# Performance work log

Hardware: AMD Instinct MI355X
Metric: run time of the kernel (lower is better)

Reference implementation:

```python
import jax, jax.numpy as jnp
import numpy as np

B, L, D, H, NB = 8, 256, 128, 4, 2
HD = D // H
N_ITEMS, TIME_SPAN = 50000, 256
EPS = 1e-8
NEG = -(2.0 ** 32) + 1.0  # torch uses -2**32+1 padding value


def _ln(x, g, b):
    m = jnp.mean(x, -1, keepdims=True)
    v = jnp.mean((x - m) ** 2, -1, keepdims=True)
    return (x - m) / jnp.sqrt(v + EPS) * g + b


def setup_inputs() -> dict:
    ks = iter(jax.random.split(jax.random.key(0), 40))

    def nrm(shape, s=0.02):
        return jax.random.normal(next(ks), shape, jnp.float32) * s

    inp = {
        "user_ids": jax.random.randint(next(ks), (B,), 0, 1000),
        "log_seqs": jax.random.randint(next(ks), (B, L), 0, N_ITEMS + 1),
        "time_matrices": jax.random.randint(next(ks), (B, L, L), 0, TIME_SPAN + 1),
        "pos_seqs": jax.random.randint(next(ks), (B, L), 1, N_ITEMS + 1),
        "neg_seqs": jax.random.randint(next(ks), (B, L), 1, N_ITEMS + 1),
    }
    inp["item_emb"] = nrm((N_ITEMS + 1, D)).at[0].set(0.0)  # padding_idx=0
    inp["posK_emb"] = nrm((L, D))
    inp["posV_emb"] = nrm((L, D))
    inp["timeK_emb"] = nrm((TIME_SPAN + 1, D))
    inp["timeV_emb"] = nrm((TIME_SPAN + 1, D))
    inp["ln1_g"] = jnp.ones((NB, D)); inp["ln1_b"] = jnp.zeros((NB, D))
    inp["Wq"] = nrm((NB, D, D)); inp["bq"] = jnp.zeros((NB, D))
    inp["Wk"] = nrm((NB, D, D)); inp["bk"] = jnp.zeros((NB, D))
    inp["Wv"] = nrm((NB, D, D)); inp["bv"] = jnp.zeros((NB, D))
    inp["ln2_g"] = jnp.ones((NB, D)); inp["ln2_b"] = jnp.zeros((NB, D))
    inp["W1"] = nrm((NB, D, D)); inp["b1"] = jnp.zeros((NB, D))
    inp["W2"] = nrm((NB, D, D)); inp["b2"] = jnp.zeros((NB, D))
    inp["lnf_g"] = jnp.ones((D,)); inp["lnf_b"] = jnp.zeros((D,))
    return inp


def reference(user_ids, log_seqs, time_matrices, pos_seqs, neg_seqs,
              item_emb, posK_emb, posV_emb, timeK_emb, timeV_emb,
              ln1_g, ln1_b, Wq, bq, Wk, bk, Wv, bv, ln2_g, ln2_b,
              W1, b1, W2, b2, lnf_g, lnf_b):
    # dropout layers are identity in eval mode
    seqs = item_emb[log_seqs] * jnp.sqrt(jnp.float32(D))          # [B,L,D]
    tK = timeK_emb[time_matrices].reshape(B, L, L, H, HD)          # [B,Lq,Lk,H,hd]
    tV = timeV_emb[time_matrices].reshape(B, L, L, H, HD)
    pad = log_seqs == 0                                            # [B,L]
    seqs = seqs * (~pad)[..., None]
    causal = jnp.triu(jnp.ones((L, L), bool), 1)                   # ~tril -> masked
    # time_mask masks by QUERY position (matches torch unsqueeze(-1).expand)
    mask = pad[:, None, :, None] | causal[None, None]              # [B,1,Lq,Lk]
    posKh = posK_emb.reshape(L, H, HD)
    posVh = posV_emb.reshape(L, H, HD)
    for i in range(NB):
        q_in = _ln(seqs, ln1_g[i], ln1_b[i])
        Qh = (q_in @ Wq[i] + bq[i]).reshape(B, L, H, HD).transpose(0, 2, 1, 3)
        Kh = (seqs @ Wk[i] + bk[i]).reshape(B, L, H, HD).transpose(0, 2, 1, 3)
        Vh = (seqs @ Wv[i] + bv[i]).reshape(B, L, H, HD).transpose(0, 2, 1, 3)
        scores = jnp.einsum("bhqd,bhkd->bhqk", Qh, Kh)
        scores = scores + jnp.einsum("bhqd,khd->bhqk", Qh, posKh)
        scores = scores + jnp.einsum("bqkhd,bhqd->bhqk", tK, Qh)
        scores = scores / jnp.sqrt(jnp.float32(HD))
        scores = jnp.where(mask, NEG, scores)
        A = jax.nn.softmax(scores, axis=-1)                        # [B,H,Lq,Lk]
        out = jnp.einsum("bhqk,bhkd->bhqd", A, Vh)
        out = out + jnp.einsum("bhqk,khd->bhqd", A, posVh)
        out = out + jnp.einsum("bhqk,bqkhd->bhqd", A, tV)
        out = out.transpose(0, 2, 1, 3).reshape(B, L, D)
        seqs = q_in + out                                          # residual on Q
        seqs = _ln(seqs, ln2_g[i], ln2_b[i])
        h = jax.nn.relu(seqs @ W1[i] + b1[i])                      # conv1d k=1 == linear
        seqs = seqs + (h @ W2[i] + b2[i])
        seqs = seqs * (~pad)[..., None]
    feats = _ln(seqs, lnf_g, lnf_b)
    pos_logits = jnp.sum(feats * item_emb[pos_seqs], -1)           # [B,L]
    neg_logits = jnp.sum(feats * item_emb[neg_seqs], -1)
    return (pos_logits, neg_logits)
```

## Files before the change

### kernel.cpp

```cpp
#include <hip/hip_runtime.h>
#include <hip/hip_bf16.h>

#define L_ 256
#define H_ 4
#define ROWS 2048
#define NEGV (-4294967295.0f)

typedef unsigned short us16;

__device__ __forceinline__ float us2f(us16 u){ return __uint_as_float(((unsigned)u)<<16); }
__device__ __forceinline__ us16 f2us(float f){ __hip_bfloat16 h=__float2bfloat16(f); return *(us16*)&h; }

__device__ __forceinline__ float dot2bf(unsigned x, unsigned y, float c){
#if __has_builtin(__builtin_amdgcn_fdot2_f32_bf16)
    typedef __bf16 bf2 __attribute__((ext_vector_type(2)));
    union U{ unsigned u; bf2 v; };
    U ux, uy; ux.u=x; uy.u=y;
    return __builtin_amdgcn_fdot2_f32_bf16(ux.v, uy.v, c, false);
#else
    float r=fmaf(us2f((us16)(x&0xffffu)), us2f((us16)(y&0xffffu)), c);
    return fmaf(us2f((us16)(x>>16)), us2f((us16)(y>>16)), r);
#endif
}

struct KArgs {
    const int *log_seqs, *tmat, *pos_seqs, *neg_seqs;
    const float *item_emb, *posK, *posV, *timeK, *timeV;
    const float *ln1g, *ln1b, *bq, *bk, *bv, *ln2g, *ln2b, *b1, *b2, *lnfg, *lnfb;
    const float *Wq, *Wk, *Wv, *W1, *W2;
    float *qin0, *qin1, *out;
    unsigned *wsP;
    us16 *tmK, *tmV, *Qb0, *Kb0, *Vb0, *Qb1, *Kb1, *Vb1;
};

__device__ __forceinline__ float gemv32(const unsigned* __restrict__ wp,
                                        const unsigned* __restrict__ xp, int c, int hk){
    float s0=0.f, s1=0.f;
    int base=hk*32;
    #pragma unroll 8
    for(int j=0;j<32;j+=2){
        s0=dot2bf(xp[base+j],   wp[(size_t)(base+j)*128+c],   s0);
        s1=dot2bf(xp[base+j+1], wp[(size_t)(base+j+1)*128+c], s1);
    }
    return s0+s1;
}

__device__ __forceinline__ void ln_rows(float* sA,
        const float* __restrict__ g, const float* __restrict__ b,
        float* qin_out, int r0, int tid){
    int r=tid>>5, l=tid&31;
    float* x=sA+r*128;
    float x0=x[l],x1=x[l+32],x2=x[l+64],x3=x[l+96];
    float s=x0+x1+x2+x3;
    #pragma unroll
    for(int o=16;o;o>>=1) s+=__shfl_xor(s,o,64);
    float m=s*(1.f/128.f);
    float d0=x0-m,d1=x1-m,d2=x2-m,d3=x3-m;
    float v=d0*d0+d1*d1+d2*d2+d3*d3;
    #pragma unroll
    for(int o=16;o;o>>=1) v+=__shfl_xor(v,o,64);
    float rstd=rsqrtf(v*(1.f/128.f)+1e-8f);
    float y0=d0*rstd*g[l]+b[l];
    float y1=d1*rstd*g[l+32]+b[l+32];
    float y2=d2*rstd*g[l+64]+b[l+64];
    float y3=d3*rstd*g[l+96]+b[l+96];
    x[l]=y0; x[l+32]=y1; x[l+64]=y2; x[l+96]=y3;
    if(qin_out){
        float* q=qin_out+(size_t)(r0+r)*128;
        q[l]=y0; q[l+32]=y1; q[l+64]=y2; q[l+96]=y3;
    }
}

__global__ __launch_bounds__(256) void k_pre(KArgs a){
    __shared__ __align__(16) float sA[1024];
    int tid=threadIdx.x, bid=blockIdx.x;
    if(bid<768){
        int m=bid>>8, rg=bid&255, r0=rg*8;
        {
            int rl=tid>>5, c4=tid&31;
            int id=a.log_seqs[r0+rl];
            float4 v=((const float4*)a.item_emb)[id*32+c4];
            float sc = id? 11.3137085f : 0.f;
            v.x*=sc; v.y*=sc; v.z*=sc; v.w*=sc;
            ((float4*)sA)[tid]=v;
        }
        __syncthreads();
        if(m==0){ ln_rows(sA, a.ln1g, a.ln1b, a.qin0, r0, tid); __syncthreads(); }
        const float* Wsrc=(m==0)?a.Wq:(m==1)?a.Wk:a.Wv;
        int cp=tid&63, rp=tid>>6, c0=2*cp, ra=2*rp, rb=ra+1;
        float a00=0,a01=0,a10=0,a11=0;
        const float* Ar=sA+ra*128;
        const float* Br=sA+rb*128;
        #pragma unroll 8
        for(int kk=0;kk<128;kk++){
            float2 wp=((const float2*)(Wsrc+(size_t)kk*128))[cp];
            float x0=Ar[kk], x1=Br[kk];
            a00=fmaf(x0,wp.x,a00); a01=fmaf(x0,wp.y,a01);
            a10=fmaf(x1,wp.x,a10); a11=fmaf(x1,wp.y,a11);
        }
        int r_a=r0+ra, r_b=r0+rb;
        if(m==0){
            float b0v=a.bq[c0], b1v=a.bq[c0+1];
            ushort2 s0; s0.x=f2us(a00+b0v); s0.y=f2us(a01+b1v);
            ushort2 s1; s1.x=f2us(a10+b0v); s1.y=f2us(a11+b1v);
            *(ushort2*)(a.Qb0+(size_t)r_a*128+c0)=s0;
            *(ushort2*)(a.Qb0+(size_t)r_b*128+c0)=s1;
        } else if(m==1){
            float b0v=a.bk[c0], b1v=a.bk[c0+1];
            int qa=r_a&255, qb2=r_b&255;
            ushort2 s0; s0.x=f2us(a00+b0v+a.posK[qa*128+c0]);  s0.y=f2us(a01+b1v+a.posK[qa*128+c0+1]);
            ushort2 s1; s1.x=f2us(a10+b0v+a.posK[qb2*128+c0]); s1.y=f2us(a11+b1v+a.posK[qb2*128+c0+1]);
            *(ushort2*)(a.Kb0+(size_t)r_a*128+c0)=s0;
            *(ushort2*)(a.Kb0+(size_t)r_b*128+c0)=s1;
        } else {
            float b0v=a.bv[c0], b1v=a.bv[c0+1];
            int qa=r_a&255, qb2=r_b&255;
            unsigned lo0=f2us(a00+b0v+a.posV[qa*128+c0]);
            unsigned lo1=f2us(a01+b1v+a.posV[qa*128+c0+1]);
            unsigned hi0=f2us(a10+b0v+a.posV[qb2*128+c0]);
            unsigned hi1=f2us(a11+b1v+a.posV[qb2*128+c0+1]);
            unsigned* Vo=(unsigned*)a.Vb0+((size_t)r_a>>1)*128;
            Vo[c0]  =lo0|(hi0<<16);
            Vo[c0+1]=lo1|(hi1<<16);
        }
    } else if(bid<880){
        int j=bid-768; int m=j>>4; int sub=j&15;
        const float* base;
        switch(m){
            case 0: base=a.W1; break;        case 1: base=a.W2; break;
            case 2: base=a.Wq+16384; break;  case 3: base=a.Wk+16384; break;
            case 4: base=a.Wv+16384; break;  case 5: base=a.W1+16384; break;
            default: base=a.W2+16384; break;
        }
        unsigned* dst=a.wsP+(size_t)m*8192;
        #pragma unroll
        for(int t2=0;t2<2;t2++){
            int o=sub*512+t2*256+tid;
            int kp=o>>7, c=o&127;
            unsigned lo=f2us(base[(size_t)(2*kp)*128+c]);
            unsigned hi=f2us(base[(size_t)(2*kp+1)*128+c]);
            dst[o]=lo|(hi<<16);
        }
    } else {
        int gi=(bid-880)*256+tid;
        if(gi<8224){
            float4 v=((const float4*)a.timeK)[gi];
            ushort4 o; o.x=f2us(v.x);o.y=f2us(v.y);o.z=f2us(v.z);o.w=f2us(v.w);
            ((ushort4*)a.tmK)[gi]=o;
        } else if(gi<16448){
            int g2=gi-8224;
            float4 v=((const float4*)a.timeV)[g2];
            ushort4 o; o.x=f2us(v.x);o.y=f2us(v.y);o.z=f2us(v.z);o.w=f2us(v.w);
            ((ushort4*)a.tmV)[g2]=o;
        }
    }
}

__global__ __launch_bounds__(512,4) void k_blk(KArgs a, int layer){
    __shared__ __align__(16) char uni[16448];
    __shared__ __align__(16) unsigned sAb[8*128];
    __shared__ __align__(16) int      sTM[512];
    __shared__ __align__(16) unsigned sQb[128];
    __shared__ __align__(16) float    sX[256];
    __shared__ __align__(16) unsigned sXb[128];
    __shared__ __align__(16) unsigned sHb[128];
    __shared__ __align__(16) unsigned sYb[128];
    __shared__ float sRed[4], sRed2[4], sRB[8];
    float* sS =(float*)uni;
    float* sPj=(float*)(uni+8192);
    float* sPr=(float*)uni;
    float* sG0=(float*)uni;
    float* sG1=(float*)(uni+2048);

    int tid=threadIdx.x, bid=blockIdx.x;
    int b=bid>>7, p=bid&127;
    int q1=p, q2=255-p, b0=b*L_;
    int r1=b0+q1, r2=b0+q2;
    bool pad1=a.log_seqs[r1]==0, pad2=a.log_seqs[r2]==0;
    const us16* Qb = layer? a.Qb1:a.Qb0;
    const us16* Kb = layer? a.Kb1:a.Kb0;
    const unsigned* Vbu = (const unsigned*)(layer? a.Vb1:a.Vb0);
    const float* qin = layer? a.qin1:a.qin0;
    const float scale=0.17677669529663687f;

    if(tid<128){
        int rowq=tid>>6, j=tid&63;
        int r=rowq?r2:r1;
        sQb[rowq*64+j]=((const unsigned*)Qb)[(size_t)r*64+j];
    }
    if(tid<256) sTM[tid]=a.tmat[(size_t)r1*L_+tid];
    else        sTM[tid]=a.tmat[(size_t)r2*L_+(tid-256)];
    __syncthreads();

    {
        int ch=tid&15, h=ch>>2;
        uint4 qv0=((const uint4*)(sQb))[ch];
        uint4 qv1=((const uint4*)(sQb+64))[ch];
        for(int t=tid>>4; t<257; t+=32){
            uint4 tv=((const uint4*)(a.tmK+(size_t)t*128))[ch];
            float p0=0.f,p1=0.f;
            p0=dot2bf(qv0.x,tv.x,p0); p0=dot2bf(qv0.y,tv.y,p0);
            p0=dot2bf(qv0.z,tv.z,p0); p0=dot2bf(qv0.w,tv.w,p0);
            p1=dot2bf(qv1.x,tv.x,p1); p1=dot2bf(qv1.y,tv.y,p1);
            p1=dot2bf(qv1.z,tv.z,p1); p1=dot2bf(qv1.w,tv.w,p1);
            p0+=__shfl_xor(p0,1,64); p0+=__shfl_xor(p0,2,64);
            p1+=__shfl_xor(p1,1,64); p1+=__shfl_xor(p1,2,64);
            if((ch&3)==0){
                sPj[t*4+h]       =p0;
                sPj[1028+t*4+h]  =p1;
            }
        }
    }
    __syncthreads();

    {
        int k=tid&255, i2=tid>>8;
        const uint4* K4=(const uint4*)(Kb+(size_t)(b0+k)*128);
        int qq=i2?q2:q1; bool pad=i2?pad2:pad1;
        int tm=sTM[i2*256+k];
        bool act=(k<=qq)&&!pad;
        float o0=NEGV,o1=NEGV,o2=NEGV,o3=NEGV;
        if(act){
            const uint4* Q4=(const uint4*)(sQb+i2*64);
            float4 pj=((const float4*)sPj)[i2*257+tm];
            float r4[4];
            #pragma unroll
            for(int h=0;h<4;h++){
                uint4 k0=K4[h*4+0],k1=K4[h*4+1],k2=K4[h*4+2],k3=K4[h*4+3];
                uint4 qa=Q4[h*4+0],qb=Q4[h*4+1],qc=Q4[h*4+2],qd=Q4[h*4+3];
                float s0=0,s1=0;
                s0=dot2bf(qa.x,k0.x,s0); s1=dot2bf(qa.y,k0.y,s1);
                s0=dot2bf(qa.z,k0.z,s0); s1=dot2bf(qa.w,k0.w,s1);
                s0=dot2bf(qb.x,k1.x,s0); s1=dot2bf(qb.y,k1.y,s1);
                s0=dot2bf(qb.z,k1.z,s0); s1=dot2bf(qb.w,k1.w,s1);
                s0=dot2bf(qc.x,k2.x,s0); s1=dot2bf(qc.y,k2.y,s1);
                s0=dot2bf(qc.z,k2.z,s0); s1=dot2bf(qc.w,k2.w,s1);
                s0=dot2bf(qd.x,k3.x,s0); s1=dot2bf(qd.y,k3.y,s1);
                s0=dot2bf(qd.z,k3.z,s0); s1=dot2bf(qd.w,k3.w,s1);
                r4[h]=s0+s1;
            }
            o0=(r4[0]+pj.x)*scale; o1=(r4[1]+pj.y)*scale;
            o2=(r4[2]+pj.z)*scale; o3=(r4[3]+pj.w)*scale;
        }
        sS[(i2*4+0)*256+k]=o0; sS[(i2*4+1)*256+k]=o1;
        sS[(i2*4+2)*256+k]=o2; sS[(i2*4+3)*256+k]=o3;
    }
    __syncthreads();

    {
        int w=tid>>6, lane=tid&63;
        int i2=w>>2, h=w&3;
        const float* row=sS+(i2*4+h)*256;
        float v0=row[lane],v1=row[lane+64],v2=row[lane+128],v3=row[lane+192];
        float mm=fmaxf(fmaxf(v0,v1),fmaxf(v2,v3));
        #pragma unroll
        for(int o=32;o;o>>=1) mm=fmaxf(mm,__shfl_xor(mm,o,64));
        float e0=__expf(v0-mm),e1=__expf(v1-mm),e2=__expf(v2-mm),e3=__expf(v3-mm);
        float ss=e0+e1+e2+e3;
        #pragma unroll
        for(int o=32;o;o>>=1) ss+=__shfl_xor(ss,o,64);
        float inv=1.f/ss;
        us16* ar=((us16*)sAb)+(i2*4+h)*256;
        ar[lane]    =f2us(e0*inv); ar[lane+64] =f2us(e1*inv);
        ar[lane+128]=f2us(e2*inv); ar[lane+192]=f2us(e3*inv);
    }
    __syncthreads();

    {
        int i2=tid>>8, s8=(tid>>4)&15, dq=tid&15;
        int qq=i2?q2:q1; bool pad=i2?pad2:pad1;
        int kend=pad?L_:qq+1;
        int k0=s8*16;
        int kmax=kend-k0; kmax=kmax<0?0:(kmax>16?16:kmax);
        int npair=(kmax+1)>>1;
        const unsigned* arow=sAb+(i2*4+(dq>>2))*128;
        const int* tmrow=sTM+i2*256;
        float ac0=0,ac1=0,ac2=0,ac3=0,ac4=0,ac5=0,ac6=0,ac7=0;
        for(int kp=0;kp<npair;kp++){
            int kx=k0+2*kp;
            unsigned aa=arow[kx>>1];
            int tma=tmrow[kx], tmb=tmrow[kx+1];
            const uint4* Vp=(const uint4*)(Vbu+((size_t)(b0+kx)>>1)*128+dq*8);
            uint4 va=Vp[0], vb4=Vp[1];
            uint4 ta=((const uint4*)(a.tmV+(size_t)tma*128))[dq];
            uint4 tb=((const uint4*)(a.tmV+(size_t)tmb*128))[dq];
            ac0=dot2bf(aa,va.x,ac0);  ac1=dot2bf(aa,va.y,ac1);
            ac2=dot2bf(aa,va.z,ac2);  ac3=dot2bf(aa,va.w,ac3);
            ac4=dot2bf(aa,vb4.x,ac4); ac5=dot2bf(aa,vb4.y,ac5);
            ac6=dot2bf(aa,vb4.z,ac6); ac7=dot2bf(aa,vb4.w,ac7);
            unsigned p0=__builtin_amdgcn_perm(tb.x,ta.x,0x05040100u);
            unsigned p1=__builtin_amdgcn_perm(tb.x,ta.x,0x07060302u);
            unsigned p2=__builtin_amdgcn_perm(tb.y,ta.y,0x05040100u);
            unsigned p3=__builtin_amdgcn_perm(tb.y,ta.y,0x07060302u);
            unsigned p4=__builtin_amdgcn_perm(tb.z,ta.z,0x05040100u);
            unsigned p5=__builtin_amdgcn_perm(tb.z,ta.z,0x07060302u);
            unsigned p6=__builtin_amdgcn_perm(tb.w,ta.w,0x05040100u);
            unsigned p7=__builtin_amdgcn_perm(tb.w,ta.w,0x07060302u);
            ac0=dot2bf(aa,p0,ac0); ac1=dot2bf(aa,p1,ac1);
            ac2=dot2bf(aa,p2,ac2); ac3=dot2bf(aa,p3,ac3);
            ac4=dot2bf(aa,p4,ac4); ac5=dot2bf(aa,p5,ac5);
            ac6=dot2bf(aa,p6,ac6); ac7=dot2bf(aa,p7,ac7);
        }
        float* dst=sPr+(i2*16+s8)*128+dq*8;
        ((float4*)dst)[0]=make_float4(ac0,ac1,ac2,ac3);
        ((float4*)dst)[1]=make_float4(ac4,ac5,ac6,ac7);
    }
    __syncthreads();

    int ii=tid>>7&1, l=tid&127;
    float v=0.f, d2v=0.f;
    if(tid<256){
        v=qin[(size_t)(ii?r2:r1)*128+l];
        #pragma unroll
        for(int sl=0;sl<16;sl++) v+=sPr[(ii*16+sl)*128+l];
        float s=v;
        #pragma unroll
        for(int o=32;o;o>>=1) s+=__shfl_xor(s,o,64);
        if((tid&63)==0) sRed[ii*2+((tid>>6)&1)]=s;
    }
    __syncthreads();
    if(tid<256){
        float m=(sRed[ii*2]+sRed[ii*2+1])*(1.f/128.f);
        d2v=v-m;
        float vv=d2v*d2v;
        #pragma unroll
        for(int o=32;o;o>>=1) vv+=__shfl_xor(vv,o,64);
        if((tid&63)==0) sRed2[ii*2+((tid>>6)&1)]=vv;
    }
    __syncthreads();
    if(tid<256){
        float rstd=rsqrtf((sRed2[ii*2]+sRed2[ii*2+1])*(1.f/128.f)+1e-8f);
        float y=d2v*rstd*a.ln2g[layer*128+l]+a.ln2b[layer*128+l];
        sX[ii*128+l]=y;
        ((us16*)sXb)[ii*128+l]=f2us(y);
    }
    __syncthreads();

    int c=tid&127, iw=(tid>>7)&1, hk=tid>>8;
    bool padw = iw? pad2:pad1;
    int  rrw  = iw? r2:r1;
    int  qw   = iw? q2:q1;
    sG0[tid]=gemv32(a.wsP+(size_t)(layer?5:0)*8192, sXb+iw*64, c, hk);
    __syncthreads();
    if(hk==0){
        float h1=sG0[tid]+sG0[tid+256]+a.b1[layer*128+c];
        ((us16*)sHb)[iw*128+c]=f2us(fmaxf(h1,0.f));
    }
    __syncthreads();
    sG1[tid]=gemv32(a.wsP+(size_t)(layer?6:1)*8192, sHb+iw*64, c, hk);
    __syncthreads();
    float f=0.f;
    if(hk==0){
        f=sG1[tid]+sG1[tid+256]+a.b2[layer*128+c]+sX[iw*128+c];
        if(padw) f=0.f;
    }

    if(layer==0){
        float d=0.f;
        if(hk==0){
            ((us16*)sYb)[iw*128+c]=f2us(f);
            float s=f;
            #pragma unroll
            for(int o=32;o;o>>=1) s+=__shfl_xor(s,o,64);
            if((tid&63)==0) sRB[iw*2+((tid>>6)&1)]=s;
        }
        __syncthreads();
        if(hk==0){
            float m=(sRB[iw*2]+sRB[iw*2+1])*(1.f/128.f);
            d=f-m;
            float vv=d*d;
            #pragma unroll
            for(int o=32;o;o>>=1) vv+=__shfl_xor(vv,o,64);
            if((tid&63)==0) sRB[4+iw*2+((tid>>6)&1)]=vv;
        }
        __syncthreads();
        if(hk==0){
            float rstd=rsqrtf((sRB[4+iw*2]+sRB[5+iw*2])*(1.f/128.f)+1e-8f);
            float y1=d*rstd*a.ln1g[128+c]+a.ln1b[128+c];
            a.qin1[(size_t)rrw*128+c]=y1;
            ((us16*)sXb)[iw*128+c]=f2us(y1);
        }
        __syncthreads();
        sG0[tid]=gemv32(a.wsP+(size_t)2*8192, sXb+iw*64, c, hk);
        __syncthreads();
        if(hk==0) a.Qb1[(size_t)rrw*128+c]=f2us(sG0[tid]+sG0[tid+256]+a.bq[128+c]);
        sG1[tid]=gemv32(a.wsP+(size_t)3*8192, sYb+iw*64, c, hk);
        __syncthreads();
        if(hk==0) a.Kb1[(size_t)rrw*128+c]=f2us(sG1[tid]+sG1[tid+256]+a.bk[128+c]+a.posK[qw*128+c]);
        sG0[tid]=gemv32(a.wsP+(size_t)4*8192, sYb+iw*64, c, hk);
        __syncthreads();
        if(hk==0) ((us16*)a.Vb1)[((size_t)rrw>>1)*256+2*c+(rrw&1)]
                    =f2us(sG0[tid]+sG0[tid+256]+a.bv[128+c]+a.posV[qw*128+c]);
    } else {
        float d=0.f;
        if(hk==0){
            float s=f;
            #pragma unroll
            for(int o=32;o;o>>=1) s+=__shfl_xor(s,o,64);
            if((tid&63)==0) sRB[iw*2+((tid>>6)&1)]=s;
        }
        __syncthreads();
        if(hk==0){
            float m=(sRB[iw*2]+sRB[iw*2+1])*(1.f/128.f);
            d=f-m;
            float vv=d*d;
            #pragma unroll
            for(int o=32;o;o>>=1) vv+=__shfl_xor(vv,o,64);
            if((tid&63)==0) sRB[4+iw*2+((tid>>6)&1)]=vv;
        }
        __syncthreads();
        if(hk==0){
            float rstd=rsqrtf((sRB[4+iw*2]+sRB[5+iw*2])*(1.f/128.f)+1e-8f);
            sX[iw*128+c]=d*rstd*a.lnfg[c]+a.lnfb[c];
        }
        __syncthreads();
        int w=tid>>6, lane=tid&63;
        if(w<4){
            int rowi=w>>1, neg=w&1;
            int rg = rowi? r2:r1;
            int id = neg? a.neg_seqs[rg] : a.pos_seqs[rg];
            const float* e=a.item_emb+(size_t)id*128;
            float s2 = sX[rowi*128+lane]*e[lane] + sX[rowi*128+lane+64]*e[lane+64];
            #pragma unroll
            for(int o=32;o;o>>=1) s2+=__shfl_xor(s2,o,64);
            if(lane==0) a.out[neg*ROWS+rg]=s2;
        }
    }
}

extern "C" void kernel_launch(void* const* d_in, const int* in_sizes, int n_in,
                              void* d_out, int out_size, void* d_ws, size_t ws_size,
                              hipStream_t stream) {
    KArgs a;
    a.log_seqs=(const int*)d_in[1];
    a.tmat    =(const int*)d_in[2];
    a.pos_seqs=(const int*)d_in[3];
    a.neg_seqs=(const int*)d_in[4];
    a.item_emb=(const float*)d_in[5];
    a.posK =(const float*)d_in[6];
    a.posV =(const float*)d_in[7];
    a.timeK=(const float*)d_in[8];
    a.timeV=(const float*)d_in[9];
    a.ln1g=(const float*)d_in[10];
    a.ln1b=(const float*)d_in[11];
    a.Wq=(const float*)d_in[12];
    a.bq=(const float*)d_in[13];
    a.Wk=(const float*)d_in[14];
    a.bk=(const float*)d_in[15];
    a.Wv=(const float*)d_in[16];
    a.bv=(const float*)d_in[17];
    a.ln2g=(const float*)d_in[18];
    a.ln2b=(const float*)d_in[19];
    a.W1=(const float*)d_in[20];
    a.b1=(const float*)d_in[21];
    a.W2=(const float*)d_in[22];
    a.b2=(const float*)d_in[23];
    a.lnfg=(const float*)d_in[24];
    a.lnfb=(const float*)d_in[25];

    const size_t MB=1u<<20;
    char* w=(char*)d_ws;
    a.qin0=(float*)(w+0*MB);
    a.qin1=(float*)(w+1*MB);
    a.Qb0 =(us16*) (w+2*MB);
    a.Kb0 =(us16*) (w+2*MB+512*1024);
    a.Vb0 =(us16*) (w+3*MB);
    a.Qb1 =(us16*) (w+3*MB+512*1024);
    a.Kb1 =(us16*) (w+4*MB);
    a.Vb1 =(us16*) (w+4*MB+512*1024);
    a.wsP =(unsigned*)(w+5*MB);
    a.tmK =(us16*) (w+5*MB+256*1024);
    a.tmV =(us16*) (w+5*MB+384*1024);
    a.out =(float*)d_out;

    k_pre<<<946,256,0,stream>>>(a);
    k_blk<<<1024,512,0,stream>>>(a,0);
    k_blk<<<1024,512,0,stream>>>(a,1);
}
```

Baseline: 206.6 us.

## Process one query row per block instead of paired causal rows

The attention/FFN block kernel now handles a single query row per 256-thread block (2048 blocks) instead of pairing rows q and 255-q in 512-thread blocks (1024 blocks). Shared memory per block halves and launch bounds move to 256x8, which should allow more resident blocks and drop the pairing index logic. In exchange the causal load balance that pairing gave is lost, so blocks for early rows finish quickly while late rows do full work. Per-row reloads of the time-K projection table also double across the grid.

After: 215.3 us. 1.04x slower.

```diff
diff --git a/kernel.cpp b/kernel.cpp
--- a/kernel.cpp
+++ b/kernel.cpp
@@ -156,73 +156,58 @@
     }
 }
 
-__global__ __launch_bounds__(512,4) void k_blk(KArgs a, int layer){
-    __shared__ __align__(16) char uni[16448];
-    __shared__ __align__(16) unsigned sAb[8*128];
-    __shared__ __align__(16) int      sTM[512];
-    __shared__ __align__(16) unsigned sQb[128];
-    __shared__ __align__(16) float    sX[256];
-    __shared__ __align__(16) unsigned sXb[128];
-    __shared__ __align__(16) unsigned sHb[128];
-    __shared__ __align__(16) unsigned sYb[128];
-    __shared__ float sRed[4], sRed2[4], sRB[8];
+__global__ __launch_bounds__(256,8) void k_blk(KArgs a, int layer){
+    __shared__ __align__(16) char uni[8224];
+    __shared__ __align__(16) unsigned sAb[4*128];
+    __shared__ __align__(16) int      sTM[256];
+    __shared__ __align__(16) unsigned sQb[64];
+    __shared__ __align__(16) float    sX[128];
+    __shared__ __align__(16) unsigned sXb[64];
+    __shared__ __align__(16) unsigned sHb[64];
+    __shared__ __align__(16) unsigned sYb[64];
+    __shared__ float sRed[2], sRed2[2], sRB[4];
     float* sS =(float*)uni;
-    float* sPj=(float*)(uni+8192);
+    float* sPj=(float*)(uni+4096);
     float* sPr=(float*)uni;
     float* sG0=(float*)uni;
-    float* sG1=(float*)(uni+2048);
+    float* sG1=(float*)(uni+1024);
 
     int tid=threadIdx.x, bid=blockIdx.x;
-    int b=bid>>7, p=bid&127;
-    int q1=p, q2=255-p, b0=b*L_;
-    int r1=b0+q1, r2=b0+q2;
-    bool pad1=a.log_seqs[r1]==0, pad2=a.log_seqs[r2]==0;
+    int b=bid>>8, q=bid&255, b0=b*L_;
+    int r=b0+q;
+    bool pad=a.log_seqs[r]==0;
     const us16* Qb = layer? a.Qb1:a.Qb0;
     const us16* Kb = layer? a.Kb1:a.Kb0;
     const unsigned* Vbu = (const unsigned*)(layer? a.Vb1:a.Vb0);
     const float* qin = layer? a.qin1:a.qin0;
     const float scale=0.17677669529663687f;
 
-    if(tid<128){
-        int rowq=tid>>6, j=tid&63;
-        int r=rowq?r2:r1;
-        sQb[rowq*64+j]=((const unsigned*)Qb)[(size_t)r*64+j];
-    }
-    if(tid<256) sTM[tid]=a.tmat[(size_t)r1*L_+tid];
-    else        sTM[tid]=a.tmat[(size_t)r2*L_+(tid-256)];
+    if(tid<64) sQb[tid]=((const unsigned*)Qb)[(size_t)r*64+tid];
+    sTM[tid]=a.tmat[(size_t)r*L_+tid];
     __syncthreads();
 
     {
-        int ch=tid&15, h=ch>>2;
-        uint4 qv0=((const uint4*)(sQb))[ch];
-        uint4 qv1=((const uint4*)(sQb+64))[ch];
-        for(int t=tid>>4; t<257; t+=32){
+        int ch=tid&15, h4=ch>>2;
+        uint4 qv=((const uint4*)sQb)[ch];
+        for(int t=tid>>4; t<257; t+=16){
             uint4 tv=((const uint4*)(a.tmK+(size_t)t*128))[ch];
-            float p0=0.f,p1=0.f;
-            p0=dot2bf(qv0.x,tv.x,p0); p0=dot2bf(qv0.y,tv.y,p0);
-            p0=dot2bf(qv0.z,tv.z,p0); p0=dot2bf(qv0.w,tv.w,p0);
-            p1=dot2bf(qv1.x,tv.x,p1); p1=dot2bf(qv1.y,tv.y,p1);
-            p1=dot2bf(qv1.z,tv.z,p1); p1=dot2bf(qv1.w,tv.w,p1);
+            float p0=0.f;
+            p0=dot2bf(qv.x,tv.x,p0); p0=dot2bf(qv.y,tv.y,p0);
+            p0=dot2bf(qv.z,tv.z,p0); p0=dot2bf(qv.w,tv.w,p0);
             p0+=__shfl_xor(p0,1,64); p0+=__shfl_xor(p0,2,64);
-            p1+=__shfl_xor(p1,1,64); p1+=__shfl_xor(p1,2,64);
-            if((ch&3)==0){
-                sPj[t*4+h]       =p0;
-                sPj[1028+t*4+h]  =p1;
-            }
+            if((ch&3)==0) sPj[t*4+h4]=p0;
         }
     }
     __syncthreads();
 
     {
-        int k=tid&255, i2=tid>>8;
+        int k=tid;
         const uint4* K4=(const uint4*)(Kb+(size_t)(b0+k)*128);
-        int qq=i2?q2:q1; bool pad=i2?pad2:pad1;
-        int tm=sTM[i2*256+k];
-        bool act=(k<=qq)&&!pad;
+        bool act=(k<=q)&&!pad;
         float o0=NEGV,o1=NEGV,o2=NEGV,o3=NEGV;
         if(act){
-            const uint4* Q4=(const uint4*)(sQb+i2*64);
-            float4 pj=((const float4*)sPj)[i2*257+tm];
+            const uint4* Q4=(const uint4*)sQb;
+            float4 pj=((const float4*)sPj)[sTM[k]];
             float r4[4];
             #pragma unroll
             for(int h=0;h<4;h++){
@@ -242,15 +227,14 @@
             o0=(r4[0]+pj.x)*scale; o1=(r4[1]+pj.y)*scale;
             o2=(r4[2]+pj.z)*scale; o3=(r4[3]+pj.w)*scale;
         }
-        sS[(i2*4+0)*256+k]=o0; sS[(i2*4+1)*256+k]=o1;
-        sS[(i2*4+2)*256+k]=o2; sS[(i2*4+3)*256+k]=o3;
+        sS[0*256+k]=o0; sS[1*256+k]=o1;
+        sS[2*256+k]=o2; sS[3*256+k]=o3;
     }
     __syncthreads();
 
     {
         int w=tid>>6, lane=tid&63;
-        int i2=w>>2, h=w&3;
-        const float* row=sS+(i2*4+h)*256;
+        const float* row=sS+w*256;
         float v0=row[lane],v1=row[lane+64],v2=row[lane+128],v3=row[lane+192];
         float mm=fmaxf(fmaxf(v0,v1),fmaxf(v2,v3));
         #pragma unroll
@@ -260,26 +244,24 @@
         #pragma unroll
         for(int o=32;o;o>>=1) ss+=__shfl_xor(ss,o,64);
         float inv=1.f/ss;
-        us16* ar=((us16*)sAb)+(i2*4+h)*256;
+        us16* ar=((us16*)sAb)+w*256;
         ar[lane]    =f2us(e0*inv); ar[lane+64] =f2us(e1*inv);
         ar[lane+128]=f2us(e2*inv); ar[lane+192]=f2us(e3*inv);
     }
     __syncthreads();
 
     {
-        int i2=tid>>8, s8=(tid>>4)&15, dq=tid&15;
-        int qq=i2?q2:q1; bool pad=i2?pad2:pad1;
-        int kend=pad?L_:qq+1;
+        int s8=tid>>4, dq=tid&15;
+        int kend=pad?L_:q+1;
         int k0=s8*16;
         int kmax=kend-k0; kmax=kmax<0?0:(kmax>16?16:kmax);
         int npair=(kmax+1)>>1;
-        const unsigned* arow=sAb+(i2*4+(dq>>2))*128;
-        const int* tmrow=sTM+i2*256;
+        const unsigned* arow=sAb+(dq>>2)*128;
         float ac0=0,ac1=0,ac2=0,ac3=0,ac4=0,ac5=0,ac6=0,ac7=0;
         for(int kp=0;kp<npair;kp++){
             int kx=k0+2*kp;
             unsigned aa=arow[kx>>1];
-            int tma=tmrow[kx], tmb=tmrow[kx+1];
+            int tma=sTM[kx], tmb=sTM[kx+1];
             const uint4* Vp=(const uint4*)(Vbu+((size_t)(b0+kx)>>1)*128+dq*8);
             uint4 va=Vp[0], vb4=Vp[1];
             uint4 ta=((const uint4*)(a.tmV+(size_t)tma*128))[dq];
@@ -301,129 +283,125 @@
             ac4=dot2bf(aa,p4,ac4); ac5=dot2bf(aa,p5,ac5);
             ac6=dot2bf(aa,p6,ac6); ac7=dot2bf(aa,p7,ac7);
         }
-        float* dst=sPr+(i2*16+s8)*128+dq*8;
+        float* dst=sPr+s8*128+dq*8;
         ((float4*)dst)[0]=make_float4(ac0,ac1,ac2,ac3);
         ((float4*)dst)[1]=make_float4(ac4,ac5,ac6,ac7);
     }
     __syncthreads();
 
-    int ii=tid>>7&1, l=tid&127;
+    int l=tid&127;
     float v=0.f, d2v=0.f;
-    if(tid<256){
-        v=qin[(size_t)(ii?r2:r1)*128+l];
-        #pragma unroll
-        for(int sl=0;sl<16;sl++) v+=sPr[(ii*16+sl)*128+l];
+    if(tid<128){
+        v=qin[(size_t)r*128+l];
+        #pragma unroll
+        for(int sl=0;sl<16;sl++) v+=sPr[sl*128+l];
         float s=v;
         #pragma unroll
         for(int o=32;o;o>>=1) s+=__shfl_xor(s,o,64);
-        if((tid&63)==0) sRed[ii*2+((tid>>6)&1)]=s;
-    }
-    __syncthreads();
-    if(tid<256){
-        float m=(sRed[ii*2]+sRed[ii*2+1])*(1.f/128.f);
+        if((tid&63)==0) sRed[tid>>6]=s;
+    }
+    __syncthreads();
+    if(tid<128){
+        float m=(sRed[0]+sRed[1])*(1.f/128.f);
         d2v=v-m;
         float vv=d2v*d2v;
         #pragma unroll
         for(int o=32;o;o>>=1) vv+=__shfl_xor(vv,o,64);
-        if((tid&63)==0) sRed2[ii*2+((tid>>6)&1)]=vv;
-    }
-    __syncthreads();
-    if(tid<256){
-        float rstd=rsqrtf((sRed2[ii*2]+sRed2[ii*2+1])*(1.f/128.f)+1e-8f);
+        if((tid&63)==0) sRed2[tid>>6]=vv;
+    }
+    __syncthreads();
+    if(tid<128){
+        float rstd=rsqrtf((sRed2[0]+sRed2[1])*(1.f/128.f)+1e-8f);
         float y=d2v*rstd*a.ln2g[layer*128+l]+a.ln2b[layer*128+l];
-        sX[ii*128+l]=y;
-        ((us16*)sXb)[ii*128+l]=f2us(y);
-    }
-    __syncthreads();
-
-    int c=tid&127, iw=(tid>>7)&1, hk=tid>>8;
-    bool padw = iw? pad2:pad1;
-    int  rrw  = iw? r2:r1;
-    int  qw   = iw? q2:q1;
-    sG0[tid]=gemv32(a.wsP+(size_t)(layer?5:0)*8192, sXb+iw*64, c, hk);
-    __syncthreads();
-    if(hk==0){
-        float h1=sG0[tid]+sG0[tid+256]+a.b1[layer*128+c];
-        ((us16*)sHb)[iw*128+c]=f2us(fmaxf(h1,0.f));
-    }
-    __syncthreads();
-    sG1[tid]=gemv32(a.wsP+(size_t)(layer?6:1)*8192, sHb+iw*64, c, hk);
+        sX[l]=y;
+        ((us16*)sXb)[l]=f2us(y);
+    }
+    __syncthreads();
+
+    int c=tid&127, hk=tid>>7;
+    sG0[tid]=gemv32(a.wsP+(size_t)(layer?5:0)*8192, sXb, c, hk);
+    __syncthreads();
+    if(tid<128){
+        float h1=sG0[c]+sG0[c+128]+a.b1[layer*128+c];
+        ((us16*)sHb)[c]=f2us(fmaxf(h1,0.f));
+    }
+    __syncthreads();
+    sG1[tid]=gemv32(a.wsP+(size_t)(layer?6:1)*8192, sHb, c, hk);
     __syncthreads();
     float f=0.f;
-    if(hk==0){
-        f=sG1[tid]+sG1[tid+256]+a.b2[layer*128+c]+sX[iw*128+c];
-        if(padw) f=0.f;
+    if(tid<128){
+        f=sG1[c]+sG1[c+128]+a.b2[layer*128+c]+sX[c];
+        if(pad) f=0.f;
     }
 
     if(layer==0){
         float d=0.f;
-        if(hk==0){
-            ((us16*)sYb)[iw*128+c]=f2us(f);
+        if(tid<128){
+            ((us16*)sYb)[l]=f2us(f);
             float s=f;
             #pragma unroll
             for(int o=32;o;o>>=1) s+=__shfl_xor(s,o,64);
-            if((tid&63)==0) sRB[iw*2+((tid>>6)&1)]=s;
-        }
-        __syncthreads();
-        if(hk==0){
-            float m=(sRB[iw*2]+sRB[iw*2+1])*(1.f/128.f);
+            if((tid&63)==0) sRB[tid>>6]=s;
+        }
+        __syncthreads();
+        if(tid<128){
+            float m=(sRB[0]+sRB[1])*(1.f/128.f);
             d=f-m;
             float vv=d*d;
             #pragma unroll
             for(int o=32;o;o>>=1) vv+=__shfl_xor(vv,o,64);
-            if((tid&63)==0) sRB[4+iw*2+((tid>>6)&1)]=vv;
-        }
-        __syncthreads();
-        if(hk==0){
-            float rstd=rsqrtf((sRB[4+iw*2]+sRB[5+iw*2])*(1.f/128.f)+1e-8f);
-            float y1=d*rstd*a.ln1g[128+c]+a.ln1b[128+c];
-            a.qin1[(size_t)rrw*128+c]=y1;
-            ((us16*)sXb)[iw*128+c]=f2us(y1);
-        }
-        __syncthreads();
-        sG0[tid]=gemv32(a.wsP+(size_t)2*8192, sXb+iw*64, c, hk);
-        __syncthreads();
-        if(hk==0) a.Qb1[(size_t)rrw*128+c]=f2us(sG0[tid]+sG0[tid+256]+a.bq[128+c]);
-        sG1[tid]=gemv32(a.wsP+(size_t)3*8192, sYb+iw*64, c, hk);
-        __syncthreads();
-        if(hk==0) a.Kb1[(size_t)rrw*128+c]=f2us(sG1[tid]+sG1[tid+256]+a.bk[128+c]+a.posK[qw*128+c]);
-        sG0[tid]=gemv32(a.wsP+(size_t)4*8192, sYb+iw*64, c, hk);
-        __syncthreads();
-        if(hk==0) ((us16*)a.Vb1)[((size_t)rrw>>1)*256+2*c+(rrw&1)]
-                    =f2us(sG0[tid]+sG0[tid+256]+a.bv[128+c]+a.posV[qw*128+c]);
+            if((tid&63)==0) sRB[2+(tid>>6)]=vv;
+        }
+        __syncthreads();
+        if(tid<128){
+            float rstd=rsqrtf((sRB[2]+sRB[3])*(1.f/128.f)+1e-8f);
+            float y1=d*rstd*a.ln1g[128+l]+a.ln1b[128+l];
+            a.qin1[(size_t)r*128+l]=y1;
+            ((us16*)sXb)[l]=f2us(y1);
+        }
+        __syncthreads();
+        sG0[tid]=gemv32(a.wsP+(size_t)2*8192, sXb, c, hk);
+        __syncthreads();
+        if(tid<128) a.Qb1[(size_t)r*128+c]=f2us(sG0[c]+sG0[c+128]+a.bq[128+c]);
+        sG1[tid]=gemv32(a.wsP+(size_t)3*8192, sYb, c, hk);
+        __syncthreads();
+        if(tid<128) a.Kb1[(size_t)r*128+c]=f2us(sG1[c]+sG1[c+128]+a.bk[128+c]+a.posK[q*128+c]);
+        sG0[tid]=gemv32(a.wsP+(size_t)4*8192, sYb, c, hk);
+        __syncthreads();
+        if(tid<128) ((us16*)a.Vb1)[((size_t)r>>1)*256+2*c+(r&1)]
+                      =f2us(sG0[c]+sG0[c+128]+a.bv[128+c]+a.posV[q*128+c]);
     } else {
         float d=0.f;
-        if(hk==0){
+        if(tid<128){
             float s=f;
             #pragma unroll
             for(int o=32;o;o>>=1) s+=__shfl_xor(s,o,64);
-            if((tid&63)==0) sRB[iw*2+((tid>>6)&1)]=s;
-        }
-        __syncthreads();
-        if(hk==0){
-            float m=(sRB[iw*2]+sRB[iw*2+1])*(1.f/128.f);
+            if((tid&63)==0) sRB[tid>>6]=s;
+        }
+        __syncthreads();
+        if(tid<128){
+            float m=(sRB[0]+sRB[1])*(1.f/128.f);
             d=f-m;
             float vv=d*d;
             #pragma unroll
             for(int o=32;o;o>>=1) vv+=__shfl_xor(vv,o,64);
-            if((tid&63)==0) sRB[4+iw*2+((tid>>6)&1)]=vv;
-        }
-        __syncthreads();
-        if(hk==0){
-            float rstd=rsqrtf((sRB[4+iw*2]+sRB[5+iw*2])*(1.f/128.f)+1e-8f);
-            sX[iw*128+c]=d*rstd*a.lnfg[c]+a.lnfb[c];
+            if((tid&63)==0) sRB[2+(tid>>6)]=vv;
+        }
+        __syncthreads();
+        if(tid<128){
+            float rstd=rsqrtf((sRB[2]+sRB[3])*(1.f/128.f)+1e-8f);
+            sX[l]=d*rstd*a.lnfg[l]+a.lnfb[l];
         }
         __syncthreads();
         int w=tid>>6, lane=tid&63;
-        if(w<4){
-            int rowi=w>>1, neg=w&1;
-            int rg = rowi? r2:r1;
-            int id = neg? a.neg_seqs[rg] : a.pos_seqs[rg];
+        if(w<2){
+            int neg=w;
+            int id = neg? a.neg_seqs[r] : a.pos_seqs[r];
             const float* e=a.item_emb+(size_t)id*128;
-            float s2 = sX[rowi*128+lane]*e[lane] + sX[rowi*128+lane+64]*e[lane+64];
+            float s2 = sX[lane]*e[lane] + sX[lane+64]*e[lane+64];
             #pragma unroll
             for(int o=32;o;o>>=1) s2+=__shfl_xor(s2,o,64);
-            if(lane==0) a.out[neg*ROWS+rg]=s2;
+            if(lane==0) a.out[neg*ROWS+r]=s2;
         }
     }
 }
@@ -474,6 +452,6 @@
     a.out =(float*)d_out;
 
     k_pre<<<946,256,0,stream>>>(a);
-    k_blk<<<1024,512,0,stream>>>(a,0);
-    k_blk<<<1024,512,0,stream>>>(a,1);
-}
+    k_blk<<<2048,256,0,stream>>>(a,0);
+    k_blk<<<2048,256,0,stream>>>(a,1);
+}
```
